# Performance work log

Hardware: AMD Instinct MI355X
Metric: run time of the kernel (lower is better)

The kernel has to match this reference:

```python
import jax, jax.numpy as jnp
import numpy as np
import math

B, S, D, H = 1, 4096, 1024, 16
DH = D // H


def setup_inputs() -> dict:
    key = jax.random.key(0)
    k1, k2, k3 = jax.random.split(key, 3)
    x = jax.random.normal(k1, (B, S, D), dtype=jnp.float32)
    # additive causal mask: 0 where allowed, -1e9 where masked (future)
    causal = jnp.tril(jnp.ones((S, S), dtype=bool))
    mask = jnp.where(causal, 0.0, -1e9).astype(jnp.float32)[None]  # [1,S,S]
    W_attn = jax.random.normal(k2, (D, 3 * D), dtype=jnp.float32) * 0.02
    b_attn = jnp.zeros((3 * D,), dtype=jnp.float32)
    W_proj = jax.random.normal(k3, (D, D), dtype=jnp.float32) * 0.02
    b_proj = jnp.zeros((D,), dtype=jnp.float32)
    return {"x": x, "mask": mask, "W_attn": W_attn, "b_attn": b_attn,
            "W_proj": W_proj, "b_proj": b_proj}


def reference(x, mask, W_attn, b_attn, W_proj, b_proj):
    # c_attn: fused QKV projection
    qkv = x @ W_attn + b_attn                      # [B,S,3D]
    q, k, v = jnp.split(qkv, 3, axis=-1)           # each [B,S,D]

    def heads(t):  # [B,S,D] -> [B,H,S,DH]
        return t.reshape(B, S, H, DH).transpose(0, 2, 1, 3)

    q, k, v = heads(q), heads(k), heads(v)
    # scores: eager O(S^2) matrix as in original
    w = jnp.einsum('bhqd,bhkd->bhqk', q, k) / math.sqrt(DH)
    w = w + mask[:, None, :, :]                    # broadcast over heads
    w = jax.nn.softmax(w, axis=-1)                 # dropout p=0 -> identity
    a = jnp.einsum('bhqk,bhkd->bhqd', w, v)        # [B,H,S,DH]
    a = a.transpose(0, 2, 1, 3).reshape(B, S, D)   # merge heads
    return a @ W_proj + b_proj
```

## Files before the change

### kernel.cpp

```cpp
#include <hip/hip_runtime.h>

typedef _Float16 half8 __attribute__((ext_vector_type(8)));
typedef short short8 __attribute__((ext_vector_type(8)));
typedef float floatx4 __attribute__((ext_vector_type(4)));

static __device__ __forceinline__ float bf2f(unsigned short u) {
  union { unsigned int u; float f; } c; c.u = ((unsigned int)u) << 16; return c.f;
}
static __device__ __forceinline__ unsigned short f2bf(float f) {
  union { float f; unsigned int u; } c; c.f = f;
  return (unsigned short)((c.u + 0x7fffu + ((c.u >> 16) & 1u)) >> 16);
}
static __device__ __forceinline__ unsigned short f2h(float f) {
  union { _Float16 h; unsigned short u; } c; c.h = (_Float16)f; return c.u;
}
static __device__ __forceinline__ unsigned int cvtpk(float a, float b) {
  unsigned int r;
  asm("v_cvt_pk_bf16_f32 %0, %1, %2" : "=v"(r) : "v"(a), "v"(b));
  return r;
}

#define GL2LDS16(gsrc, ldst)                                                        \
  __builtin_amdgcn_global_load_lds(                                                 \
      (const __attribute__((address_space(1))) void*)(const void*)(gsrc),           \
      (__attribute__((address_space(3))) void*)(void*)(ldst), 16, 0, 0)

static __device__ __forceinline__ int dtype_bf16(const unsigned short* mask16) {
  return mask16[1] != 0;
}

__global__ __launch_bounds__(256) void k_prep(const void* __restrict__ x,
    const void* __restrict__ Wa, const void* __restrict__ Wp,
    const unsigned short* __restrict__ mask16, _Float16* __restrict__ xh,
    _Float16* __restrict__ WaT, _Float16* __restrict__ WpT) {
  __shared__ float tile[64 * 65];
  const int dt = dtype_bf16(mask16);
  const int bx = blockIdx.x;
  const int tid = threadIdx.x;
  if (bx < 4096) {
    const int i = (bx * 256 + tid) * 4;
    _Float16 o[4];
    if (dt) {
      ushort4 u = *((const ushort4*)((const unsigned short*)x + i));
      o[0] = (_Float16)bf2f(u.x); o[1] = (_Float16)bf2f(u.y);
      o[2] = (_Float16)bf2f(u.z); o[3] = (_Float16)bf2f(u.w);
    } else {
      float4 f = *((const float4*)((const float*)x + i));
      o[0] = (_Float16)f.x; o[1] = (_Float16)f.y;
      o[2] = (_Float16)f.z; o[3] = (_Float16)f.w;
    }
    union { _Float16 h[4]; uint2 u; } pk;
    pk.h[0] = o[0]; pk.h[1] = o[1]; pk.h[2] = o[2]; pk.h[3] = o[3];
    *((uint2*)(xh + i)) = pk.u;
    return;
  }
  const void* in; _Float16* out; int n0, k0, N;
  if (bx < 4864) { const int b = bx - 4096; in = Wa; out = WaT; N = 3072;
                   n0 = (b % 48) * 64; k0 = (b / 48) * 64; }
  else           { const int b = bx - 4864; in = Wp; out = WpT; N = 1024;
                   n0 = (b % 16) * 64; k0 = (b / 16) * 64; }
  const int r = tid >> 2;
#pragma unroll
  for (int it = 0; it < 4; ++it) {
    const int c4 = (tid & 3) + it * 4;
    const size_t src = (size_t)(k0 + r) * N + n0 + c4 * 4;
    float v[4];
    if (dt) {
      ushort4 u = *((const ushort4*)((const unsigned short*)in + src));
      v[0] = bf2f(u.x); v[1] = bf2f(u.y); v[2] = bf2f(u.z); v[3] = bf2f(u.w);
    } else {
      float4 f = *((const float4*)((const float*)in + src));
      v[0] = f.x; v[1] = f.y; v[2] = f.z; v[3] = f.w;
    }
#pragma unroll
    for (int jj = 0; jj < 4; ++jj) tile[r * 65 + c4 * 4 + jj] = v[jj];
  }
  __syncthreads();
#pragma unroll
  for (int it = 0; it < 4; ++it) {
    const int rn = (tid >> 4) + it * 16;
    const int kc = tid & 15;
    union { _Float16 h[4]; uint2 u; } pk;
#pragma unroll
    for (int jj = 0; jj < 4; ++jj)
      pk.h[jj] = (_Float16)tile[(kc * 4 + jj) * 65 + rn];
    *(uint2*)(out + (size_t)(n0 + rn) * 1024 + k0 + kc * 4) = pk.u;
  }
}

template <int KD>
static __device__ __forceinline__ void gemm_mainloop(const _Float16* __restrict__ A,
    const _Float16* __restrict__ Bt, int m0, int n0,
    _Float16* As, _Float16* Bs, floatx4 acc[4][4]) {
  const int tid = threadIdx.x;
  const int wave = tid >> 6, lane = tid & 63;
  const int lq = lane & 15, quad = lane >> 4;
  const int wm = (wave >> 1) * 64, wn = (wave & 1) * 64;
  const int scol = (lane & 3) * 8;
  for (int k0 = 0; k0 < KD; k0 += 32) {
    __syncthreads();
#pragma unroll
    for (int op = 0; op < 2; ++op) {
      const int rbase = wave * 32 + op * 16;
      const int row = rbase + (lane >> 2);
      GL2LDS16(A + (size_t)(m0 + row) * KD + k0 + scol, As + rbase * 32);
      GL2LDS16(Bt + (size_t)(n0 + row) * KD + k0 + scol, Bs + rbase * 32);
    }
    __builtin_amdgcn_s_waitcnt(0x0f70);
    __syncthreads();
    half8 af[4], bf[4];
#pragma unroll
    for (int i = 0; i < 4; ++i) {
      af[i] = *(const half8*)(As + (wm + i * 16 + lq) * 32 + quad * 8);
      bf[i] = *(const half8*)(Bs + (wn + i * 16 + lq) * 32 + quad * 8);
    }
#pragma unroll
    for (int i = 0; i < 4; ++i)
#pragma unroll
      for (int j = 0; j < 4; ++j)
        acc[i][j] = __builtin_amdgcn_mfma_f32_16x16x32_f16(af[i], bf[j], acc[i][j], 0, 0, 0);
  }
}

__global__ __launch_bounds__(256, 1) void k_gemm_qkv(const _Float16* __restrict__ A,
    const _Float16* __restrict__ Bt, const void* __restrict__ bias,
    const unsigned short* __restrict__ mask16, _Float16* __restrict__ Qb,
    _Float16* __restrict__ Kb, unsigned short* __restrict__ VTb) {
  __shared__ __attribute__((aligned(16))) unsigned short smem[128 * 136];
  _Float16* As = (_Float16*)smem;
  _Float16* Bs = As + 4096;
  const int tid = threadIdx.x, wave = tid >> 6, lane = tid & 63;
  const int lq = lane & 15, quad = lane >> 4;
  const int m0 = blockIdx.y * 128, n0 = blockIdx.x * 128;
  const int wm = (wave >> 1) * 64, wn = (wave & 1) * 64;
  floatx4 acc[4][4] = {};
  gemm_mainloop<1024>(A, Bt, m0, n0, As, Bs, acc);
  const int dt = dtype_bf16(mask16);
  const int sec = n0 >> 10;
  const float scale = (sec == 0) ? 0.1803368801f : 1.0f;
  __syncthreads();
#pragma unroll
  for (int i = 0; i < 4; ++i) {
    const int lmb = wm + i * 16 + quad * 4;
#pragma unroll
    for (int j = 0; j < 4; ++j) {
      const int ln = wn + j * 16 + lq;
      const int gcol = n0 + ln;
      const float bv = dt ? bf2f(((const unsigned short*)bias)[gcol])
                          : ((const float*)bias)[gcol];
#pragma unroll
      for (int r = 0; r < 4; ++r) {
        const float v = (acc[i][j][r] + bv) * scale;
        const unsigned short bits = (sec == 2) ? f2bf(v) : f2h(v);
        if (sec == 2) smem[ln * 136 + lmb + r] = bits;
        else          smem[(lmb + r) * 136 + ln] = bits;
      }
    }
  }
  __syncthreads();
  if (sec == 2) {
#pragma unroll
    for (int it = 0; it < 8; ++it) {
      const int row = (tid >> 4) + it * 16;
      const int ch = tid & 15;
      const uint4 v = *(const uint4*)&smem[row * 136 + ch * 8];
      *(uint4*)(VTb + (size_t)(n0 + row - 2048) * 4096 + m0 + ch * 8) = v;
    }
  } else {
    _Float16* dst = (sec == 0) ? Qb : Kb;
#pragma unroll
    for (int it = 0; it < 8; ++it) {
      const int row = (tid >> 4) + it * 16;
      const int ch = tid & 15;
      const uint4 v = *(const uint4*)&smem[row * 136 + ch * 8];
      const int c = (n0 & 1023) + ch * 8;
      const int hh = c >> 6, dh = c & 63;
      *(uint4*)(dst + ((size_t)(hh * 4096 + m0 + row)) * 64 + dh) = v;
    }
  }
}

__global__ __launch_bounds__(256, 2) void k_attn(const _Float16* __restrict__ Qb,
    const _Float16* __restrict__ Kb, const unsigned short* __restrict__ VTb,
    unsigned short* __restrict__ Op0, unsigned short* __restrict__ Op1,
    unsigned short* __restrict__ Op2, unsigned short* __restrict__ Op3,
    float* __restrict__ Lp) {
  constexpr int S = 4096;
  const int bx = blockIdx.x;
  const int h  = bx & 15;
  const int pr = (bx >> 4) & 7;
  const int cj = bx >> 7;
  const int kbg = 15 - pr;
  const int ksm = pr;
  const int sB  = 64 - 4 * pr;
  const int fb  = sB / 17;
  const int p0 = cj * 17, p1 = p0 + 17;
  const int tid = threadIdx.x, wave = tid >> 6, lane = tid & 63;
  const int lq = lane & 15, quad = lane >> 4;
  __shared__ __attribute__((aligned(16))) _Float16 Ks[64 * 72];
  __shared__ __attribute__((aligned(16))) unsigned short VTs[64 * 72];
  const _Float16* Qh = Qb + (size_t)h * S * 64;
  const _Float16* Kh = Kb + (size_t)h * S * 64;
  const unsigned short* VTh = VTb + (size_t)h * 64 * S;
  short8 aones;
#pragma unroll
  for (int jj = 0; jj < 8; ++jj) aones[jj] = (short)0x3F80;
  const int srow = tid >> 2, schunk = (tid & 3) * 16;

#define LOADQ()                                                                     \
  {                                                                                 \
    const int qb0 = 256 * ku + wave * 64;                                           \
    _Pragma("unroll")                                                               \
    for (int m = 0; m < 4; ++m)                                                     \
      _Pragma("unroll")                                                             \
      for (int ch = 0; ch < 2; ++ch)                                                \
        qf[m][ch] = *(const half8*)(Qh + (size_t)(qb0 + m * 16 + lq) * 64           \
                                    + ch * 32 + quad * 8);                          \
  }
#define ZEROACC()                                                                   \
  {                                                                                 \
    _Pragma("unroll")                                                               \
    for (int nf = 0; nf < 4; ++nf)                                                  \
      _Pragma("unroll")                                                             \
      for (int m = 0; m < 4; ++m) o[nf][m] = (floatx4){0.f, 0.f, 0.f, 0.f};         \
    _Pragma("unroll")                                                               \
    for (int m = 0; m < 4; ++m) ol[m] = (floatx4){0.f, 0.f, 0.f, 0.f};              \
  }
#define EPILOGUE(SLOT)                                                              \
  {                                                                                 \
    const int sl = (SLOT);                                                          \
    unsigned short* Ob = sl == 0 ? Op0 : sl == 1 ? Op1 : sl == 2 ? Op2 : Op3;       \
    const int r0 = sl << 10;                                                        \
    const int qb0 = 256 * ku + wave * 64;                                           \
    _Pragma("unroll")                                                               \
    for (int m = 0; m < 4; ++m) {                                                   \
      const int q = qb0 + m * 16 + lq;                                              \
      _Pragma("unroll")                                                             \
      for (int nf = 0; nf < 4; ++nf) {                                              \
        union { unsigned short u[4]; uint2 v; } pk;                                 \
        _Pragma("unroll")                                                           \
        for (int r = 0; r < 4; ++r) pk.u[r] = f2bf(o[nf][m][r]);                    \
        *(uint2*)(Ob + (size_t)(q - r0) * 1024 + h * 64 + nf * 16 + quad * 4) =     \
            pk.v;                                                                   \
      }                                                                             \
      if (quad == 0) Lp[sl * 65536 + h * 4096 + q] = ol[m][0];                      \
    }                                                                               \
  }

  int ku = (p0 < sB) ? kbg : ksm;
  half8 qf[4][2];
  floatx4 o[4][4];
  floatx4 ol[4];
  LOADQ();
  ZEROACC();
  uint4 kreg0, kreg1, vreg0, vreg1;
  {
    const int t0 = (p0 < sB) ? p0 : p0 - sB;
    const int kt = t0 * 64;
    kreg0 = *(const uint4*)(Kh + (size_t)(kt + srow) * 64 + schunk);
    kreg1 = *(const uint4*)(Kh + (size_t)(kt + srow) * 64 + schunk + 8);
    vreg0 = *(const uint4*)(VTh + (size_t)srow * S + kt + schunk);
    vreg1 = *(const uint4*)(VTh + (size_t)srow * S + kt + schunk + 8);
  }
  for (int pos = p0; pos < p1; ++pos) {
    if (pos == sB) {
      EPILOGUE(cj);
      ku = ksm;
      LOADQ();
      ZEROACC();
    }
    const int t = (pos < sB) ? pos : pos - sB;
    const int kt = t * 64;
    __syncthreads();
    *(uint4*)(Ks + srow * 72 + schunk) = kreg0;
    *(uint4*)(Ks + srow * 72 + schunk + 8) = kreg1;
    *(uint4*)(VTs + srow * 72 + schunk) = vreg0;
    *(uint4*)(VTs + srow * 72 + schunk + 8) = vreg1;
    __syncthreads();
    if (pos + 1 < p1) {
      const int nx = pos + 1;
      const int tn = (nx < sB) ? nx : nx - sB;
      const int kn = tn * 64;
      kreg0 = *(const uint4*)(Kh + (size_t)(kn + srow) * 64 + schunk);
      kreg1 = *(const uint4*)(Kh + (size_t)(kn + srow) * 64 + schunk + 8);
      vreg0 = *(const uint4*)(VTh + (size_t)srow * S + kn + schunk);
      vreg1 = *(const uint4*)(VTh + (size_t)srow * S + kn + schunk + 8);
    }
    const int qb0 = 256 * ku + wave * 64;
    if ((wave >= 2) || (t < 4 * ku + 2)) {
#pragma unroll
      for (int c = 0; c < 2; ++c) {
        floatx4 sc[4][2];
        {
          half8 kf0[2], kf1[2];
#pragma unroll
          for (int kb = 0; kb < 2; ++kb) {
            const int row = (c * 2 + kb) * 16 + lq;
            kf0[kb] = *(const half8*)(Ks + row * 72 + quad * 8);
            kf1[kb] = *(const half8*)(Ks + row * 72 + 32 + quad * 8);
          }
          __builtin_amdgcn_s_setprio(1);
#pragma unroll
          for (int m = 0; m < 4; ++m)
#pragma unroll
            for (int kb = 0; kb < 2; ++kb) {
              floatx4 z = {0.f, 0.f, 0.f, 0.f};
              z = __builtin_amdgcn_mfma_f32_16x16x32_f16(kf0[kb], qf[m][0], z, 0, 0, 0);
              sc[m][kb] = __builtin_amdgcn_mfma_f32_16x16x32_f16(kf1[kb], qf[m][1], z, 0, 0, 0);
            }
          __builtin_amdgcn_s_setprio(0);
        }
        short8 pf[4];
#pragma unroll
        for (int m = 0; m < 4; ++m) {
          unsigned int dw0, dw1, dw2, dw3;
          if (kt + c * 32 + 31 > qb0 + m * 16) {
            const int q = qb0 + m * 16 + lq;
            float pv0[4], pv1[4];
#pragma unroll
            for (int r = 0; r < 4; ++r) {
              const int key0 = kt + (c * 2 + 0) * 16 + quad * 4 + r;
              const int key1 = kt + (c * 2 + 1) * 16 + quad * 4 + r;
              const float e0 = __builtin_amdgcn_exp2f(sc[m][0][r]);
              const float e1 = __builtin_amdgcn_exp2f(sc[m][1][r]);
              pv0[r] = (key0 > q) ? 0.f : e0;
              pv1[r] = (key1 > q) ? 0.f : e1;
            }
            dw0 = cvtpk(pv0[0], pv0[1]); dw1 = cvtpk(pv0[2], pv0[3]);
            dw2 = cvtpk(pv1[0], pv1[1]); dw3 = cvtpk(pv1[2], pv1[3]);
          } else {
            float pv0[4], pv1[4];
#pragma unroll
            for (int r = 0; r < 4; ++r) {
              pv0[r] = __builtin_amdgcn_exp2f(sc[m][0][r]);
              pv1[r] = __builtin_amdgcn_exp2f(sc[m][1][r]);
            }
            dw0 = cvtpk(pv0[0], pv0[1]); dw1 = cvtpk(pv0[2], pv0[3]);
            dw2 = cvtpk(pv1[0], pv1[1]); dw3 = cvtpk(pv1[2], pv1[3]);
          }
          asm("v_permlane32_swap_b32 %0, %1" : "+v"(dw0), "+v"(dw2));
          asm("v_permlane32_swap_b32 %0, %1" : "+v"(dw1), "+v"(dw3));
          asm("v_permlane16_swap_b32 %0, %1" : "+v"(dw0), "+v"(dw2));
          asm("v_permlane16_swap_b32 %0, %1" : "+v"(dw1), "+v"(dw3));
          union { unsigned int d[4]; short8 s; } u;
          u.d[0] = dw0; u.d[1] = dw1; u.d[2] = dw2; u.d[3] = dw3;
          pf[m] = u.s;
        }
        __builtin_amdgcn_s_setprio(1);
#pragma unroll
        for (int nf = 0; nf < 4; ++nf) {
          const short8 vfr = *(const short8*)(VTs + (nf * 16 + lq) * 72 + c * 32 + quad * 8);
#pragma unroll
          for (int m = 0; m < 4; ++m)
            o[nf][m] = __builtin_amdgcn_mfma_f32_16x16x32_bf16(vfr, pf[m], o[nf][m], 0, 0, 0);
        }
#pragma unroll
        for (int m = 0; m < 4; ++m)
          ol[m] = __builtin_amdgcn_mfma_f32_16x16x32_bf16(aones, pf[m], ol[m], 0, 0, 0);
        __builtin_amdgcn_s_setprio(0);
      }
    }
  }
  EPILOGUE((p1 <= sB) ? cj : cj - fb);
#undef LOADQ
#undef ZEROACC
#undef EPILOGUE
}

__global__ __launch_bounds__(256) void k_merge(const unsigned short* __restrict__ Op0,
    const unsigned short* __restrict__ Op1, const unsigned short* __restrict__ Op2,
    const unsigned short* __restrict__ Op3, const float* __restrict__ Lp,
    _Float16* __restrict__ Ah) {
  const int row = blockIdx.x;
  const int c = threadIdx.x * 4;
  const int h = c >> 6;
  const int k = row >> 8;
  const int n = (k >= 8) ? (4 * k + 20) / 17 : 4 - (64 - 4 * k) / 17;
  float l = 0.f, v0 = 0.f, v1 = 0.f, v2 = 0.f, v3 = 0.f;
#pragma unroll
  for (int s = 0; s < 4; ++s) {
    if (s < n) {
      const unsigned short* Ob = s == 0 ? Op0 : s == 1 ? Op1 : s == 2 ? Op2 : Op3;
      l += Lp[s * 65536 + h * 4096 + row];
      const ushort4 a = *(const ushort4*)(Ob + (size_t)(row - (s << 10)) * 1024 + c);
      v0 += bf2f(a.x); v1 += bf2f(a.y); v2 += bf2f(a.z); v3 += bf2f(a.w);
    }
  }
  const float inv = __builtin_amdgcn_rcpf(l);
  union { _Float16 h4[4]; uint2 u; } pk;
  pk.h4[0] = (_Float16)(v0 * inv);
  pk.h4[1] = (_Float16)(v1 * inv);
  pk.h4[2] = (_Float16)(v2 * inv);
  pk.h4[3] = (_Float16)(v3 * inv);
  *(uint2*)(Ah + (size_t)row * 1024 + c) = pk.u;
}

__global__ __launch_bounds__(256, 1) void k_gemm_proj(const _Float16* __restrict__ A,
    const _Float16* __restrict__ Bt, const void* __restrict__ bias,
    const unsigned short* __restrict__ mask16, void* __restrict__ out) {
  __shared__ __attribute__((aligned(16))) _Float16 As[64 * 32];
  __shared__ __attribute__((aligned(16))) _Float16 Bs[128 * 32];
  const int tid = threadIdx.x, wave = tid >> 6, lane = tid & 63;
  const int lq = lane & 15, quad = lane >> 4;
  const int m0 = blockIdx.y * 64, n0 = blockIdx.x * 128;
  const int wm = (wave >> 1) * 32, wn = (wave & 1) * 64;
  const int scol = (lane & 3) * 8;
  floatx4 acc[2][4] = {};
  for (int k0 = 0; k0 < 1024; k0 += 32) {
    __syncthreads();
    {
      const int arow = wave * 16 + (lane >> 2);
      GL2LDS16(A + (size_t)(m0 + arow) * 1024 + k0 + scol, As + wave * 16 * 32);
#pragma unroll
      for (int op = 0; op < 2; ++op) {
        const int rbase = wave * 32 + op * 16;
        const int row = rbase + (lane >> 2);
        GL2LDS16(Bt + (size_t)(n0 + row) * 1024 + k0 + scol, Bs + rbase * 32);
      }
    }
    __builtin_amdgcn_s_waitcnt(0x0f70);
    __syncthreads();
    half8 af[2], bf[4];
#pragma unroll
    for (int i = 0; i < 2; ++i)
      af[i] = *(const half8*)(As + (wm + i * 16 + lq) * 32 + quad * 8);
#pragma unroll
    for (int j = 0; j < 4; ++j)
      bf[j] = *(const half8*)(Bs + (wn + j * 16 + lq) * 32 + quad * 8);
#pragma unroll
    for (int i = 0; i < 2; ++i)
#pragma unroll
      for (int j = 0; j < 4; ++j)
        acc[i][j] = __builtin_amdgcn_mfma_f32_16x16x32_f16(af[i], bf[j], acc[i][j], 0, 0, 0);
  }
  const int dt = dtype_bf16(mask16);
#pragma unroll
  for (int i = 0; i < 2; ++i) {
    const int growb = m0 + wm + i * 16 + quad * 4;
#pragma unroll
    for (int j = 0; j < 4; ++j) {
      const int gcol = n0 + wn + j * 16 + lq;
      const float bv = dt ? bf2f(((const unsigned short*)bias)[gcol])
                          : ((const float*)bias)[gcol];
#pragma unroll
      for (int r = 0; r < 4; ++r) {
        const float v = acc[i][j][r] + bv;
        if (dt) ((unsigned short*)out)[(size_t)(growb + r) * 1024 + gcol] = f2bf(v);
        else    ((float*)out)[(size_t)(growb + r) * 1024 + gcol] = v;
      }
    }
  }
}

extern "C" void kernel_launch(void* const* d_in, const int* in_sizes, int n_in,
                              void* d_out, int out_size, void* d_ws, size_t ws_size,
                              hipStream_t stream) {
  const void* x    = d_in[0];
  const unsigned short* mask16 = (const unsigned short*)d_in[1];
  const void* Wa   = d_in[2];
  const void* ba   = d_in[3];
  const void* Wp   = d_in[4];
  const void* bp   = d_in[5];
  char* ws = (char*)d_ws;
  _Float16* WpT       = (_Float16*)(ws + 0);
  _Float16* WaT       = (_Float16*)(ws + 2097152);
  float*    Lp        = (float*)   (ws + 2097152);
  unsigned short* Op2 = (unsigned short*)(ws + 3145728);
  _Float16* xh        = (_Float16*)(ws + 8388608);
  unsigned short* Op0 = (unsigned short*)(ws + 8388608);
  _Float16* Qb        = (_Float16*)(ws + 16777216);
  _Float16* Ah        = (_Float16*)(ws + 16777216);
  _Float16* Kb        = (_Float16*)(ws + 25165824);
  unsigned short* VTb = (unsigned short*)(ws + 33554432);
  unsigned short* Op1 = (unsigned short*)(ws + 41943040);
  unsigned short* Op3 = (unsigned short*)(ws + 48234496);

  k_prep<<<5120, 256, 0, stream>>>(x, Wa, Wp, mask16, xh, WaT, WpT);
  { dim3 g(24, 32); k_gemm_qkv<<<g, 256, 0, stream>>>(xh, WaT, ba, mask16, Qb, Kb, VTb); }
  k_attn<<<512, 256, 0, stream>>>(Qb, Kb, VTb, Op0, Op1, Op2, Op3, Lp);
  k_merge<<<4096, 256, 0, stream>>>(Op0, Op1, Op2, Op3, Lp, Ah);
  { dim3 g(8, 64);  k_gemm_proj<<<g, 256, 0, stream>>>(Ah, WpT, bp, mask16, d_out); }
}
```

Before: 238.9 us.

## Fuse split-KV merge into output projection GEMM A-tile loading

```diff
diff --git a/kernel.cpp b/kernel.cpp
--- a/kernel.cpp
+++ b/kernel.cpp
@@ -367,59 +367,72 @@
 #undef EPILOGUE
 }
 
-__global__ __launch_bounds__(256) void k_merge(const unsigned short* __restrict__ Op0,
+__global__ __launch_bounds__(256, 1) void k_gemm_proj(const unsigned short* __restrict__ Op0,
     const unsigned short* __restrict__ Op1, const unsigned short* __restrict__ Op2,
     const unsigned short* __restrict__ Op3, const float* __restrict__ Lp,
-    _Float16* __restrict__ Ah) {
-  const int row = blockIdx.x;
-  const int c = threadIdx.x * 4;
-  const int h = c >> 6;
-  const int k = row >> 8;
-  const int n = (k >= 8) ? (4 * k + 20) / 17 : 4 - (64 - 4 * k) / 17;
-  float l = 0.f, v0 = 0.f, v1 = 0.f, v2 = 0.f, v3 = 0.f;
-#pragma unroll
-  for (int s = 0; s < 4; ++s) {
-    if (s < n) {
-      const unsigned short* Ob = s == 0 ? Op0 : s == 1 ? Op1 : s == 2 ? Op2 : Op3;
-      l += Lp[s * 65536 + h * 4096 + row];
-      const ushort4 a = *(const ushort4*)(Ob + (size_t)(row - (s << 10)) * 1024 + c);
-      v0 += bf2f(a.x); v1 += bf2f(a.y); v2 += bf2f(a.z); v3 += bf2f(a.w);
-    }
-  }
-  const float inv = __builtin_amdgcn_rcpf(l);
-  union { _Float16 h4[4]; uint2 u; } pk;
-  pk.h4[0] = (_Float16)(v0 * inv);
-  pk.h4[1] = (_Float16)(v1 * inv);
-  pk.h4[2] = (_Float16)(v2 * inv);
-  pk.h4[3] = (_Float16)(v3 * inv);
-  *(uint2*)(Ah + (size_t)row * 1024 + c) = pk.u;
-}
-
-__global__ __launch_bounds__(256, 1) void k_gemm_proj(const _Float16* __restrict__ A,
     const _Float16* __restrict__ Bt, const void* __restrict__ bias,
     const unsigned short* __restrict__ mask16, void* __restrict__ out) {
   __shared__ __attribute__((aligned(16))) _Float16 As[64 * 32];
   __shared__ __attribute__((aligned(16))) _Float16 Bs[128 * 32];
+  __shared__ float Linv[16 * 64];
   const int tid = threadIdx.x, wave = tid >> 6, lane = tid & 63;
   const int lq = lane & 15, quad = lane >> 4;
   const int m0 = blockIdx.y * 64, n0 = blockIdx.x * 128;
   const int wm = (wave >> 1) * 32, wn = (wave & 1) * 64;
   const int scol = (lane & 3) * 8;
+  const int ku = m0 >> 8;
+  const int n = (ku >= 8) ? (4 * ku + 20) / 17 : 4 - (64 - 4 * ku) / 17;
+#pragma unroll
+  for (int i = 0; i < 4; ++i) {
+    const int e = tid + i * 256;
+    const int hh = e >> 6, row = e & 63;
+    float l = 0.f;
+#pragma unroll
+    for (int s = 0; s < 4; ++s)
+      if (s < n) l += Lp[s * 65536 + hh * 4096 + m0 + row];
+    Linv[e] = __builtin_amdgcn_rcpf(l);
+  }
+  const int arow = wave * 16 + (lane >> 2);
+  const int achk = (lane & 3) * 8;
+  uint4 ra[4];
+#define LOADA(K0)                                                                   \
+  {                                                                                 \
+    _Pragma("unroll")                                                               \
+    for (int s = 0; s < 4; ++s)                                                     \
+      if (s < n) {                                                                  \
+        const unsigned short* Ob = s == 0 ? Op0 : s == 1 ? Op1 : s == 2 ? Op2 : Op3;\
+        ra[s] = *(const uint4*)(Ob + (size_t)(m0 + arow - (s << 10)) * 1024 +       \
+                                (K0) + achk);                                       \
+      }                                                                             \
+  }
+  LOADA(0);
   floatx4 acc[2][4] = {};
   for (int k0 = 0; k0 < 1024; k0 += 32) {
     __syncthreads();
+#pragma unroll
+    for (int op = 0; op < 2; ++op) {
+      const int rbase = wave * 32 + op * 16;
+      const int row = rbase + (lane >> 2);
+      GL2LDS16(Bt + (size_t)(n0 + row) * 1024 + k0 + scol, Bs + rbase * 32);
+    }
     {
-      const int arow = wave * 16 + (lane >> 2);
-      GL2LDS16(A + (size_t)(m0 + arow) * 1024 + k0 + scol, As + wave * 16 * 32);
-#pragma unroll
-      for (int op = 0; op < 2; ++op) {
-        const int rbase = wave * 32 + op * 16;
-        const int row = rbase + (lane >> 2);
-        GL2LDS16(Bt + (size_t)(n0 + row) * 1024 + k0 + scol, Bs + rbase * 32);
-      }
+      float v[8] = {0.f, 0.f, 0.f, 0.f, 0.f, 0.f, 0.f, 0.f};
+#pragma unroll
+      for (int s = 0; s < 4; ++s)
+        if (s < n) {
+          union { uint4 q; unsigned short u[8]; } cv; cv.q = ra[s];
+#pragma unroll
+          for (int j = 0; j < 8; ++j) v[j] += bf2f(cv.u[j]);
+        }
+      const float inv = Linv[(k0 >> 6) * 64 + arow];
+      union { _Float16 h[8]; uint4 q; } pk;
+#pragma unroll
+      for (int j = 0; j < 8; ++j) pk.h[j] = (_Float16)(v[j] * inv);
+      *(uint4*)(As + arow * 32 + achk) = pk.q;
     }
     __builtin_amdgcn_s_waitcnt(0x0f70);
     __syncthreads();
+    if (k0 + 32 < 1024) LOADA(k0 + 32);
     half8 af[2], bf[4];
 #pragma unroll
     for (int i = 0; i < 2; ++i)
@@ -433,6 +446,7 @@
       for (int j = 0; j < 4; ++j)
         acc[i][j] = __builtin_amdgcn_mfma_f32_16x16x32_f16(af[i], bf[j], acc[i][j], 0, 0, 0);
   }
+#undef LOADA
   const int dt = dtype_bf16(mask16);
 #pragma unroll
   for (int i = 0; i < 2; ++i) {
@@ -469,7 +483,6 @@
   _Float16* xh        = (_Float16*)(ws + 8388608);
   unsigned short* Op0 = (unsigned short*)(ws + 8388608);
   _Float16* Qb        = (_Float16*)(ws + 16777216);
-  _Float16* Ah        = (_Float16*)(ws + 16777216);
   _Float16* Kb        = (_Float16*)(ws + 25165824);
   unsigned short* VTb = (unsigned short*)(ws + 33554432);
   unsigned short* Op1 = (unsigned short*)(ws + 41943040);
@@ -478,6 +491,5 @@
   k_prep<<<5120, 256, 0, stream>>>(x, Wa, Wp, mask16, xh, WaT, WpT);
   { dim3 g(24, 32); k_gemm_qkv<<<g, 256, 0, stream>>>(xh, WaT, ba, mask16, Qb, Kb, VTb); }
   k_attn<<<512, 256, 0, stream>>>(Qb, Kb, VTb, Op0, Op1, Op2, Op3, Lp);
-  k_merge<<<4096, 256, 0, stream>>>(Op0, Op1, Op2, Op3, Lp, Ah);
-  { dim3 g(8, 64);  k_gemm_proj<<<g, 256, 0, stream>>>(Ah, WpT, bp, mask16, d_out); }
-}
+  { dim3 g(8, 64);  k_gemm_proj<<<g, 256, 0, stream>>>(Op0, Op1, Op2, Op3, Lp, WpT, bp, mask16, d_out); }
+}
```

Result: slower. 247.8 us (+3.7%).
